# Performance work log

Hardware: AMD Instinct MI355X
Metric: run time of the kernel (lower is better)

Reference implementation:

```python
import jax, jax.numpy as jnp
import numpy as np

BSZ, IN_DIM, OUT_DIM = 512, 1024, 2048
M_AND = 5        # Anderson memory (self.m)
BETA = 1.0
LAM = 1e-4
ALPHA = 1.0
TOL = 1e-5
MAX_ITER = 50
M_MON = 1.0      # monotonicity parameter of MONSingleFc


def _multiply(A, B, z):
    # MONSingleFc.multiply: (1-m)z - z A^T A + z B^T - z B
    Az = z @ A.T
    return (1.0 - M_MON) * z - Az @ A + z @ B.T - z @ B


def _relu(z):
    return jnp.maximum(z, 0.0)


def _single_it(A, B, z, bias):
    zn = _multiply(A, B, z)
    zn = (1.0 - ALPHA) * z + ALPHA * (zn + bias)
    zn = _relu(zn)
    err = jnp.linalg.norm(zn - z) / (1e-6 + jnp.linalg.norm(zn))
    return zn, err


def _anderson_solve(A, B, bias):
    bsz, d = bias.shape
    dt = bias.dtype
    Z = jnp.zeros((bsz, M_AND, d), dt)
    F = jnp.zeros((bsz, M_AND, d), dt)
    z0 = jnp.zeros((bsz, d), dt)
    f0, _ = _single_it(A, B, z0, bias)
    F = F.at[:, 0].set(f0)
    Z = Z.at[:, 1].set(f0)
    f1, _ = _single_it(A, B, f0, bias)
    F = F.at[:, 1].set(f1)
    eye = jnp.eye(M_AND, dtype=dt)

    def cond(s):
        Z, F, it, err = s
        return (it < MAX_ITER) & (err > TOL)

    def body(s):
        Z, F, it, _ = s
        n = jnp.minimum(M_AND, it)
        mask = jnp.arange(M_AND) < n                         # active Anderson slots
        # For it < m the unused slots of Z and F are still zero, so G = F - Z
        # has zero rows there and GGt's Frobenius norm matches the :n slice.
        G = F - Z                                            # (bsz, m, d)
        GGt = jnp.einsum('bmd,bnd->bmn', G, G)
        nrm = jnp.linalg.norm(GGt.reshape(GGt.shape[0], -1), axis=-1)
        GGt = GGt / (nrm[:, None, None] + 1e-6)
        pair = mask[:, None] & mask[None, :]
        # identity padding on inactive slots keeps the solve well-posed and
        # yields alpha = 0 there, equivalent to slicing [:n+1, :n+1].
        Hb = jnp.where(pair, GGt + LAM * eye, eye)
        mk = mask.astype(dt)
        H = jnp.zeros((bsz, M_AND + 1, M_AND + 1), dt)
        H = H.at[:, 0, 1:].set(mk).at[:, 1:, 0].set(mk).at[:, 1:, 1:].set(Hb)
        y = jnp.zeros((bsz, M_AND + 1, 1), dt).at[:, 0, 0].set(1.0)
        alpha = jnp.linalg.solve(H, y)[:, 1:, 0]             # (bsz, m)
        z_new = BETA * jnp.einsum('bm,bmd->bd', alpha, F) \
              + (1.0 - BETA) * jnp.einsum('bm,bmd->bd', alpha, Z)
        slot = it % M_AND
        Z = Z.at[:, slot].set(z_new)
        zo, err = _single_it(A, B, z_new, bias)
        F = F.at[:, slot].set(zo)
        return Z, F, it + 1, err

    Z, F, it, err = jax.lax.while_loop(
        cond, body, (Z, F, jnp.array(2, jnp.int32), jnp.array(jnp.inf, dt)))
    slot = (it - 1) % M_AND
    return Z[:, slot]


def setup_inputs():
    key = jax.random.key(0)
    kx, ka, kb, kw, kub = jax.random.split(key, 5)
    s = 1.0 / np.sqrt(OUT_DIM).astype(np.float32)
    x = jax.random.normal(kx, (BSZ, IN_DIM), jnp.float32)
    # scaled so ||W|| < 1 -> forward-backward splitting converges (trained MON regime)
    A = 0.3 * s * jax.random.normal(ka, (OUT_DIM, OUT_DIM), jnp.float32)
    B = 0.1 * s * jax.random.normal(kb, (OUT_DIM, OUT_DIM), jnp.float32)
    U_W = (1.0 / np.sqrt(IN_DIM).astype(np.float32)) * jax.random.normal(kw, (OUT_DIM, IN_DIM), jnp.float32)
    U_b = 0.01 * jax.random.normal(kub, (OUT_DIM,), jnp.float32)
    return {"x": x, "A": A, "B": B, "U_W": U_W, "U_b": U_b}


def reference(x, A, B, U_W, U_b):
    bias = x @ U_W.T + U_b                       # linear_module.bias(x)
    z_star = _anderson_solve(A, B, bias)         # equilibrium (no-grad in torch)
    zn = _relu(_multiply(A, B, z_star) + bias)   # final full step: nonlin(linear(x, z*))
    return zn
```

## Files before the change

### kernel.cpp

```cpp
#include <hip/hip_runtime.h>
#include <hip/hip_bf16.h>
#include <math.h>

#define BSZ      512
#define IN_DIM   1024
#define OUT_DIM  2048
#define M_AND    5
#define LAM      1e-4f
#define TOL      1e-5f
#define MAX_ITER 50
#define SPLIT_IT 24
#define NBLK     256

typedef __bf16 bf16x8 __attribute__((ext_vector_type(8)));
typedef float  f32x4  __attribute__((ext_vector_type(4)));
typedef unsigned short u16x8 __attribute__((ext_vector_type(8)));
typedef unsigned short u16x4 __attribute__((ext_vector_type(4)));
typedef __hip_bfloat16 bf16;

#define GAS __attribute__((address_space(1)))
#define LAS __attribute__((address_space(3)))

union BU { bf16 b; unsigned short u; };

__device__ __forceinline__ float bf2f(unsigned short u) {
    union { unsigned int i; float f; } c; c.i = (unsigned int)u << 16; return c.f;
}
__device__ __forceinline__ unsigned short f2bf(float f) {
    BU t; t.b = __float2bfloat16(f); return t.u;
}

static constexpr size_t BIAS_B = 0;
static constexpr size_t F_B    = BIAS_B + (size_t)BSZ * OUT_DIM * 4;
static constexpr size_t G_B    = F_B    + (size_t)BSZ * M_AND * OUT_DIM * 4;
static constexpr size_t ZH_B   = G_B    + (size_t)BSZ * M_AND * OUT_DIM * 2;
static constexpr size_t ZL_B   = ZH_B   + (size_t)BSZ * OUT_DIM * 2;
static constexpr size_t XH_B   = ZL_B   + (size_t)BSZ * OUT_DIM * 2;
static constexpr size_t XL_B   = XH_B   + (size_t)BSZ * IN_DIM * 2;
static constexpr size_t UH_B   = XL_B   + (size_t)BSZ * IN_DIM * 2;
static constexpr size_t UL_B   = UH_B   + (size_t)OUT_DIM * IN_DIM * 2;
static constexpr size_t AT_B   = UL_B   + (size_t)OUT_DIM * IN_DIM * 2;
static constexpr size_t WT_B   = AT_B   + (size_t)OUT_DIM * OUT_DIM * 2;
static constexpr size_t RED_B  = WT_B   + (size_t)OUT_DIM * OUT_DIM * 2;
static constexpr size_t BAR_B  = RED_B  + 512;
static constexpr size_t CTR_B  = BAR_B  + 64;
static constexpr size_t FLAG_B = CTR_B  + 256;
static constexpr size_t CTRL_SZ = 512 + 64 + 256 + 16;

template<int ROUNDS>
__device__ __forceinline__ void stage_tile(const void* __restrict__ g0, int row_bytes,
                                           void* l0, int tid)
{
    #pragma unroll
    for (int q = 0; q < ROUNDS; ++q) {
        const int D   = q * 4096 + tid * 16;
        const int r   = D >> 7;
        const int cb  = D & 127;
        const int scb = cb ^ ((r & 7) << 4);
        const char* gsrc = (const char*)g0 + (size_t)r * row_bytes + scb;
        char* ldst = (char*)l0 + q * 4096 + (tid >> 6) * 1024;
        __builtin_amdgcn_global_load_lds((const GAS void*)gsrc, (LAS void*)ldst, 16, 0, 0);
    }
}

__device__ __forceinline__ bf16x8 read_frag(const void* tile, int row, int cb)
{
    return *(const bf16x8*)((const char*)tile + row * 128 + (cb ^ ((row & 7) << 4)));
}

__device__ __forceinline__ void gsync(unsigned int* bar)
{
    __syncthreads();
    if (threadIdx.x == 0) {
        __threadfence();
        const unsigned int g =
            __hip_atomic_load(&bar[1], __ATOMIC_ACQUIRE, __HIP_MEMORY_SCOPE_AGENT);
        const unsigned int a =
            __hip_atomic_fetch_add(&bar[0], 1u, __ATOMIC_ACQ_REL, __HIP_MEMORY_SCOPE_AGENT);
        if (a == NBLK - 1) {
            __hip_atomic_store(&bar[0], 0u, __ATOMIC_RELAXED, __HIP_MEMORY_SCOPE_AGENT);
            __hip_atomic_fetch_add(&bar[1], 1u, __ATOMIC_RELEASE, __HIP_MEMORY_SCOPE_AGENT);
        } else {
            while (__hip_atomic_load(&bar[1], __ATOMIC_ACQUIRE, __HIP_MEMORY_SCOPE_AGENT) == g)
                __builtin_amdgcn_s_sleep(1);
        }
        __threadfence();
    }
    __syncthreads();
}

__global__ __launch_bounds__(256)
void conv_hilo(const float* __restrict__ src, bf16* __restrict__ h, bf16* __restrict__ l)
{
    const size_t i4 = ((size_t)blockIdx.x * 256 + threadIdx.x) * 4;
    const float4 v = *(const float4*)&src[i4];
    const float vv[4] = {v.x, v.y, v.z, v.w};
    union { short4 s4; unsigned short u[4]; } ph, pl;
    #pragma unroll
    for (int j = 0; j < 4; ++j) {
        ph.u[j] = f2bf(vv[j]);
        pl.u[j] = f2bf(vv[j] - bf2f(ph.u[j]));
    }
    *(short4*)((char*)h + i4 * 2) = ph.s4;
    *(short4*)((char*)l + i4 * 2) = pl.s4;
}

__global__ __launch_bounds__(256)
void prep_at(const float* __restrict__ A, bf16* __restrict__ At)
{
    __shared__ float t[64][65];
    const int tid = threadIdx.x;
    const int k0 = blockIdx.y * 64, c0 = blockIdx.x * 64;
    const int cc = tid & 63, rr = tid >> 6;
    #pragma unroll
    for (int q = 0; q < 16; ++q)
        t[rr + 4 * q][cc] = A[(size_t)(k0 + rr + 4 * q) * OUT_DIM + c0 + cc];
    __syncthreads();
    #pragma unroll
    for (int q = 0; q < 16; ++q)
        At[(size_t)(c0 + rr + 4 * q) * OUT_DIM + k0 + cc] = __float2bfloat16(t[cc][rr + 4 * q]);
}

__global__ __launch_bounds__(256)
void w_mfma(const bf16* __restrict__ At, const float* __restrict__ Bm, bf16* __restrict__ Wt)
{
    __shared__ __align__(16) bf16 lds[2][2][64 * 64];
    const int tid = threadIdx.x;
    const int lane = tid & 63, wid = tid >> 6;
    const int wy = wid >> 1, wx = wid & 1;

    int bb = blockIdx.x;
    int ti = (int)((sqrtf(8.f * bb + 1.f) - 1.f) * 0.5f);
    while ((ti + 1) * (ti + 2) / 2 <= bb) ++ti;
    while (ti * (ti + 1) / 2 > bb) --ti;
    const int tj = bb - ti * (ti + 1) / 2;
    const int r0 = ti * 64, c0 = tj * 64;
    const bool diag = (ti == tj);

    f32x4 acc[2][2];
    #pragma unroll
    for (int i = 0; i < 2; ++i)
        #pragma unroll
        for (int j = 0; j < 2; ++j) acc[i][j] = 0;

    stage_tile<2>(At + (size_t)r0 * OUT_DIM, OUT_DIM * 2, lds[0][0], tid);
    stage_tile<2>(At + (size_t)c0 * OUT_DIM, OUT_DIM * 2, lds[0][1], tid);
    __syncthreads();
    int cur = 0;
    for (int t = 0; t < 32; ++t) {
        if (t + 1 < 32) {
            const int kk = (t + 1) * 64;
            stage_tile<2>(At + (size_t)r0 * OUT_DIM + kk, OUT_DIM * 2, lds[cur ^ 1][0], tid);
            stage_tile<2>(At + (size_t)c0 * OUT_DIM + kk, OUT_DIM * 2, lds[cur ^ 1][1], tid);
        }
        const bf16* Ta = lds[cur][0];
        const bf16* Tb = lds[cur][1];
        #pragma unroll
        for (int kf = 0; kf < 2; ++kf) {
            const int cb = kf * 64 + (lane >> 4) * 16;
            bf16x8 bfr[2];
            #pragma unroll
            for (int nj = 0; nj < 2; ++nj)
                bfr[nj] = read_frag(Tb, wx * 32 + nj * 16 + (lane & 15), cb);
            #pragma unroll
            for (int mi = 0; mi < 2; ++mi) {
                bf16x8 afr = read_frag(Ta, wy * 32 + mi * 16 + (lane & 15), cb);
                #pragma unroll
                for (int nj = 0; nj < 2; ++nj)
                    acc[mi][nj] = __builtin_amdgcn_mfma_f32_16x16x32_bf16(afr, bfr[nj], acc[mi][nj], 0, 0, 0);
            }
        }
        __syncthreads();
        cur ^= 1;
    }

    #pragma unroll
    for (int mi = 0; mi < 2; ++mi) {
        const int rb = r0 + wy * 32 + mi * 16 + (lane >> 4) * 4;
        #pragma unroll
        for (int nj = 0; nj < 2; ++nj) {
            const int c = c0 + wx * 32 + nj * 16 + (lane & 15);
            const float4 bc = *(const float4*)&Bm[(size_t)c * OUT_DIM + rb];
            const float bcv[4] = {bc.x, bc.y, bc.z, bc.w};
            union { short4 s4; unsigned short u[4]; } p;
            #pragma unroll
            for (int g = 0; g < 4; ++g) {
                const float a = acc[mi][nj][g];
                const float brc = Bm[(size_t)(rb + g) * OUT_DIM + c];
                const float w = bcv[g] - brc - a;
                p.u[g] = f2bf(w);
                if (!diag) {
                    const float wm = brc - bcv[g] - a;
                    *((unsigned short*)Wt + (size_t)(rb + g) * OUT_DIM + c) = f2bf(wm);
                }
            }
            *(short4*)((char*)Wt + ((size_t)c * OUT_DIM + rb) * 2) = p.s4;
        }
    }
}

__global__ __launch_bounds__(256)
void bias_mfma(const bf16* __restrict__ xh, const bf16* __restrict__ xl,
               const bf16* __restrict__ uh, const bf16* __restrict__ ul,
               const float* __restrict__ Ub, float* __restrict__ bias,
               float* __restrict__ F, unsigned short* __restrict__ G,
               unsigned short* __restrict__ zh, unsigned short* __restrict__ zl)
{
    __shared__ __align__(16) bf16 lds[2][4][64 * 64];
    const int tid = threadIdx.x;
    const int lane = tid & 63, wid = tid >> 6;
    const int wy = wid >> 1, wx = wid & 1;
    const int m0 = blockIdx.y * 64, n0 = blockIdx.x * 64;

    f32x4 acc[2][2];
    #pragma unroll
    for (int i = 0; i < 2; ++i)
        #pragma unroll
        for (int j = 0; j < 2; ++j) acc[i][j] = 0;

    stage_tile<2>(xh + (size_t)m0 * IN_DIM, IN_DIM * 2, lds[0][0], tid);
    stage_tile<2>(xl + (size_t)m0 * IN_DIM, IN_DIM * 2, lds[0][1], tid);
    stage_tile<2>(uh + (size_t)n0 * IN_DIM, IN_DIM * 2, lds[0][2], tid);
    stage_tile<2>(ul + (size_t)n0 * IN_DIM, IN_DIM * 2, lds[0][3], tid);
    __syncthreads();
    int cur = 0;
    for (int t = 0; t < 16; ++t) {
        if (t + 1 < 16) {
            const int kk = (t + 1) * 64;
            stage_tile<2>(xh + (size_t)m0 * IN_DIM + kk, IN_DIM * 2, lds[cur ^ 1][0], tid);
            stage_tile<2>(xl + (size_t)m0 * IN_DIM + kk, IN_DIM * 2, lds[cur ^ 1][1], tid);
            stage_tile<2>(uh + (size_t)n0 * IN_DIM + kk, IN_DIM * 2, lds[cur ^ 1][2], tid);
            stage_tile<2>(ul + (size_t)n0 * IN_DIM + kk, IN_DIM * 2, lds[cur ^ 1][3], tid);
        }
        const bf16* Txh = lds[cur][0];
        const bf16* Txl = lds[cur][1];
        const bf16* Tuh = lds[cur][2];
        const bf16* Tul = lds[cur][3];
        #pragma unroll
        for (int kf = 0; kf < 2; ++kf) {
            const int cb = kf * 64 + (lane >> 4) * 16;
            bf16x8 bh[2], bl[2];
            #pragma unroll
            for (int nj = 0; nj < 2; ++nj) {
                const int br = wx * 32 + nj * 16 + (lane & 15);
                bh[nj] = read_frag(Tuh, br, cb);
                bl[nj] = read_frag(Tul, br, cb);
            }
            #pragma unroll
            for (int mi = 0; mi < 2; ++mi) {
                const int ar = wy * 32 + mi * 16 + (lane & 15);
                bf16x8 ah = read_frag(Txh, ar, cb);
                bf16x8 al = read_frag(Txl, ar, cb);
                #pragma unroll
                for (int nj = 0; nj < 2; ++nj) {
                    acc[mi][nj] = __builtin_amdgcn_mfma_f32_16x16x32_bf16(ah, bh[nj], acc[mi][nj], 0, 0, 0);
                    acc[mi][nj] = __builtin_amdgcn_mfma_f32_16x16x32_bf16(ah, bl[nj], acc[mi][nj], 0, 0, 0);
                    acc[mi][nj] = __builtin_amdgcn_mfma_f32_16x16x32_bf16(al, bh[nj], acc[mi][nj], 0, 0, 0);
                }
            }
        }
        __syncthreads();
        cur ^= 1;
    }

    #pragma unroll
    for (int mi = 0; mi < 2; ++mi) {
        const int mb = m0 + wy * 32 + mi * 16 + (lane >> 4) * 4;
        #pragma unroll
        for (int nj = 0; nj < 2; ++nj) {
            const int n = n0 + wx * 32 + nj * 16 + (lane & 15);
            const float ub = Ub[n];
            #pragma unroll
            for (int g = 0; g < 4; ++g) {
                const int m = mb + g;
                const size_t idx = (size_t)m * OUT_DIM + n;
                const float v = acc[mi][nj][g] + ub;
                bias[idx] = v;
                const float f = fmaxf(v, 0.f);
                F[((size_t)m * M_AND + 0) * OUT_DIM + n] = f;
                G[((size_t)m * M_AND + 0) * OUT_DIM + n] = f2bf(f);
                const unsigned short h = f2bf(f);
                zh[idx] = h;
                zl[idx] = f2bf(f - bf2f(h));
            }
        }
    }
}

template<bool DO_ERR>
__device__ __forceinline__ void iter_core(
    const int m0, const int n0, const int tid,
    const unsigned short* __restrict__ zh, const unsigned short* __restrict__ zl,
    const bf16* __restrict__ Wt, const float* __restrict__ bias,
    float* __restrict__ F, unsigned short* __restrict__ G, float* __restrict__ out,
    float* red, bf16* lds_buf, const int slot, const int it)
{
    const int lane = tid & 63, wid = tid >> 6;
    const int wy = wid >> 1, wx = wid & 1;
    #define BUFP(c,i) (lds_buf + ((c) * 3 + (i)) * 4096)

    f32x4 acc[2][2];
    #pragma unroll
    for (int i = 0; i < 2; ++i)
        #pragma unroll
        for (int j = 0; j < 2; ++j) acc[i][j] = 0;

    stage_tile<2>(zh + (size_t)m0 * OUT_DIM, OUT_DIM * 2, BUFP(0, 0), tid);
    stage_tile<2>(zl + (size_t)m0 * OUT_DIM, OUT_DIM * 2, BUFP(0, 1), tid);
    stage_tile<2>(Wt + (size_t)n0 * OUT_DIM, OUT_DIM * 2, BUFP(0, 2), tid);
    __syncthreads();
    int cur = 0;
    for (int t = 0; t < 32; ++t) {
        if (t + 1 < 32) {
            const int kk = (t + 1) * 64;
            stage_tile<2>(zh + (size_t)m0 * OUT_DIM + kk, OUT_DIM * 2, BUFP(cur ^ 1, 0), tid);
            stage_tile<2>(zl + (size_t)m0 * OUT_DIM + kk, OUT_DIM * 2, BUFP(cur ^ 1, 1), tid);
            stage_tile<2>(Wt + (size_t)n0 * OUT_DIM + kk, OUT_DIM * 2, BUFP(cur ^ 1, 2), tid);
        }
        const bf16* Th = BUFP(cur, 0);
        const bf16* Tl = BUFP(cur, 1);
        const bf16* Tw = BUFP(cur, 2);
        #pragma unroll
        for (int kf = 0; kf < 2; ++kf) {
            const int cb = kf * 64 + (lane >> 4) * 16;
            bf16x8 bfr[2];
            #pragma unroll
            for (int nj = 0; nj < 2; ++nj)
                bfr[nj] = read_frag(Tw, wx * 32 + nj * 16 + (lane & 15), cb);
            #pragma unroll
            for (int mi = 0; mi < 2; ++mi) {
                const int rrow = wy * 32 + mi * 16 + (lane & 15);
                bf16x8 ah = read_frag(Th, rrow, cb);
                bf16x8 al = read_frag(Tl, rrow, cb);
                #pragma unroll
                for (int nj = 0; nj < 2; ++nj) {
                    acc[mi][nj] = __builtin_amdgcn_mfma_f32_16x16x32_bf16(ah, bfr[nj], acc[mi][nj], 0, 0, 0);
                    acc[mi][nj] = __builtin_amdgcn_mfma_f32_16x16x32_bf16(al, bfr[nj], acc[mi][nj], 0, 0, 0);
                }
            }
        }
        __syncthreads();
        cur ^= 1;
    }
    #undef BUFP

    float lnum = 0.f, lden = 0.f;
    #pragma unroll
    for (int mi = 0; mi < 2; ++mi) {
        const int mb = m0 + wy * 32 + mi * 16 + (lane >> 4) * 4;
        #pragma unroll
        for (int nj = 0; nj < 2; ++nj) {
            const int n = n0 + wx * 32 + nj * 16 + (lane & 15);
            #pragma unroll
            for (int g = 0; g < 4; ++g) {
                const int m = mb + g;
                const size_t idx = (size_t)m * OUT_DIM + n;
                float v = acc[mi][nj][g] + bias[idx];
                v = fmaxf(v, 0.f);
                const float zc = bf2f(zh[idx]) + bf2f(zl[idx]);
                const float gg = v - zc;
                F[((size_t)m * M_AND + slot) * OUT_DIM + n] = v;
                G[((size_t)m * M_AND + slot) * OUT_DIM + n] = f2bf(gg);
                out[idx] = v;
                if (DO_ERR) { lnum += gg * gg; lden += v * v; }
            }
        }
    }

    if (DO_ERR) {
        #pragma unroll
        for (int off = 32; off; off >>= 1) {
            lnum += __shfl_down(lnum, off);
            lden += __shfl_down(lden, off);
        }
        __shared__ float swn[4], swd[4];
        if ((tid & 63) == 0) { swn[tid >> 6] = lnum; swd[tid >> 6] = lden; }
        __syncthreads();
        if (tid == 0) {
            atomicAdd(&red[2 * it],     swn[0] + swn[1] + swn[2] + swn[3]);
            atomicAdd(&red[2 * it + 1], swd[0] + swd[1] + swd[2] + swd[3]);
        }
    }
}

template<bool DO_ERR>
__global__ __launch_bounds__(256)
void iter_mfma(const unsigned short* __restrict__ zh, const unsigned short* __restrict__ zl,
               const bf16* __restrict__ Wt, const float* __restrict__ bias,
               float* __restrict__ F, unsigned short* __restrict__ G, float* __restrict__ out,
               float* red, unsigned int* ctr, int* flag, int slot, int it)
{
    if (((volatile int*)flag)[0]) return;
    __shared__ __align__(16) bf16 lds_buf[2 * 3 * 4096];
    iter_core<DO_ERR>(blockIdx.y * 64, blockIdx.x * 64, threadIdx.x,
                      zh, zl, Wt, bias, F, G, out, red, lds_buf, slot, it);
    if (DO_ERR && threadIdx.x == 0) {
        __threadfence();
        const unsigned int done = atomicAdd(&ctr[it], 1u);
        if (done == 256 - 1) {
            const float num2 = ((volatile float*)red)[2 * it];
            const float den2 = ((volatile float*)red)[2 * it + 1];
            if (sqrtf(num2) <= TOL * (1e-6f + sqrtf(den2)))
                ((volatile int*)flag)[0] = 1;
        }
    }
}

__global__ __launch_bounds__(512)
void anderson_kernel(const float* __restrict__ F, const unsigned short* __restrict__ G,
                     unsigned short* __restrict__ zh, unsigned short* __restrict__ zl,
                     int* flag, int it)
{
    if (((volatile int*)flag)[0]) return;
    const int b = blockIdx.x;
    const int tid = threadIdx.x;
    const int lane = tid & 63, wid = tid >> 6;
    const int n = (it < M_AND) ? it : M_AND;
    const int c0 = tid * 4;
    const unsigned short* Gb = G + (size_t)b * M_AND * OUT_DIM;
    const float* Fb = F + (size_t)b * M_AND * OUT_DIM;

    float g[M_AND][4];
    float4 f[M_AND];
    #pragma unroll
    for (int m = 0; m < M_AND; ++m) {
        f[m] = *(const float4*)(Fb + (size_t)m * OUT_DIM + c0);
        if (m < n) {
            const u16x4 gv = *(const u16x4*)(Gb + (size_t)m * OUT_DIM + c0);
            #pragma unroll
            for (int q = 0; q < 4; ++q) g[m][q] = bf2f(gv[q]);
        } else {
            #pragma unroll
            for (int q = 0; q < 4; ++q) g[m][q] = 0.f;
        }
    }

    float dots[15];
    {
        int p = 0;
        #pragma unroll
        for (int i = 0; i < M_AND; ++i)
            #pragma unroll
            for (int j = i; j < M_AND; ++j) {
                float s = 0.f;
                #pragma unroll
                for (int q = 0; q < 4; ++q) s += g[i][q] * g[j][q];
                dots[p++] = s;
            }
    }

    __shared__ float sred[15][8];
    #pragma unroll
    for (int p = 0; p < 15; ++p) {
        float v = dots[p];
        #pragma unroll
        for (int off = 32; off; off >>= 1) v += __shfl_xor(v, off);
        if (lane == 0) sred[p][wid] = v;
    }
    __syncthreads();

    __shared__ float s_alpha[M_AND];
    if (tid == 0) {
        float GGm[M_AND][M_AND];
        int p = 0;
        for (int i = 0; i < M_AND; ++i)
            for (int j = i; j < M_AND; ++j) {
                float v = 0.f;
                for (int w = 0; w < 8; ++w) v += sred[p][w];
                GGm[i][j] = v; GGm[j][i] = v; ++p;
            }
        float fro = 0.f;
        for (int i = 0; i < M_AND; ++i)
            for (int j = 0; j < M_AND; ++j) fro += GGm[i][j] * GGm[i][j];
        const float inv = 1.f / (sqrtf(fro) + 1e-6f);

        float Mm[M_AND][M_AND];
        for (int i = 0; i < n; ++i)
            for (int j = 0; j < n; ++j)
                Mm[i][j] = GGm[i][j] * inv + (i == j ? LAM : 0.f);

        float L[M_AND][M_AND];
        for (int i = 0; i < n; ++i)
            for (int j = 0; j <= i; ++j) {
                float s = Mm[i][j];
                for (int k = 0; k < j; ++k) s -= L[i][k] * L[j][k];
                L[i][j] = (i == j) ? sqrtf(fmaxf(s, 1e-20f)) : s / L[j][j];
            }
        float y[M_AND], u[M_AND];
        for (int i = 0; i < n; ++i) {
            float s = 1.f;
            for (int k = 0; k < i; ++k) s -= L[i][k] * y[k];
            y[i] = s / L[i][i];
        }
        for (int i = n - 1; i >= 0; --i) {
            float s = y[i];
            for (int k = i + 1; k < n; ++k) s -= L[k][i] * u[k];
            u[i] = s / L[i][i];
        }
        float su = 0.f;
        for (int i = 0; i < n; ++i) su += u[i];
        const float isu = 1.f / su;
        for (int m = 0; m < M_AND; ++m) s_alpha[m] = (m < n) ? u[m] * isu : 0.f;
    }
    __syncthreads();

    float z[4] = {};
    #pragma unroll
    for (int m = 0; m < M_AND; ++m) {
        if (m < n) {
            const float a = s_alpha[m];
            z[0] += a * f[m].x; z[1] += a * f[m].y;
            z[2] += a * f[m].z; z[3] += a * f[m].w;
        }
    }
    u16x4 hv, lv;
    #pragma unroll
    for (int q = 0; q < 4; ++q) {
        const unsigned short h = f2bf(z[q]);
        hv[q] = h;
        lv[q] = f2bf(z[q] - bf2f(h));
    }
    *(u16x4*)(zh + (size_t)b * OUT_DIM + c0) = hv;
    *(u16x4*)(zl + (size_t)b * OUT_DIM + c0) = lv;
}

__global__ __launch_bounds__(256)
void tail_loop(unsigned short* zh, unsigned short* zl,
               const bf16* __restrict__ Wt, const float* __restrict__ bias,
               float* F, unsigned short* G, float* out,
               float* red, unsigned int* bar, int* flag)
{
    if (((volatile int*)flag)[0]) return;
    __shared__ __align__(16) bf16 lds_buf[2 * 3 * 4096];
    __shared__ float sred2[2][2][15];
    __shared__ float s_alpha[2][M_AND];
    const int bid = blockIdx.x, tid = threadIdx.x;

    for (int it = SPLIT_IT; it < MAX_ITER; ++it) {
        {
            const int half = tid >> 7, lt = tid & 127;
            const int r = bid * 2 + half;
            const int wv = lt >> 6;
            const unsigned short* Gb = G + (size_t)r * M_AND * OUT_DIM;
            const float* Fb = F + (size_t)r * M_AND * OUT_DIM;
            const int c0 = lt * 16;

            float g[M_AND][16];
            #pragma unroll
            for (int m = 0; m < M_AND; ++m) {
                const u16x8 ga = *(const u16x8*)(Gb + (size_t)m * OUT_DIM + c0);
                const u16x8 gb2 = *(const u16x8*)(Gb + (size_t)m * OUT_DIM + c0 + 8);
                #pragma unroll
                for (int q = 0; q < 8; ++q) { g[m][q] = bf2f(ga[q]); g[m][8 + q] = bf2f(gb2[q]); }
            }
            {
                int p = 0;
                #pragma unroll
                for (int i = 0; i < M_AND; ++i)
                    #pragma unroll
                    for (int j = i; j < M_AND; ++j) {
                        float s = 0.f;
                        #pragma unroll
                        for (int q = 0; q < 16; ++q) s += g[i][q] * g[j][q];
                        float v = s;
                        #pragma unroll
                        for (int off = 32; off; off >>= 1) v += __shfl_xor(v, off);
                        if ((lt & 63) == 0) sred2[half][wv][p] = v;
                        ++p;
                    }
            }
            __syncthreads();
            if (lt == 0) {
                float GGm[M_AND][M_AND];
                int p = 0;
                for (int i = 0; i < M_AND; ++i)
                    for (int j = i; j < M_AND; ++j) {
                        const float v = sred2[half][0][p] + sred2[half][1][p];
                        GGm[i][j] = v; GGm[j][i] = v; ++p;
                    }
                float fro = 0.f;
                for (int i = 0; i < M_AND; ++i)
                    for (int j = 0; j < M_AND; ++j) fro += GGm[i][j] * GGm[i][j];
                const float inv = 1.f / (sqrtf(fro) + 1e-6f);
                float Mm[M_AND][M_AND];
                for (int i = 0; i < M_AND; ++i)
                    for (int j = 0; j < M_AND; ++j)
                        Mm[i][j] = GGm[i][j] * inv + (i == j ? LAM : 0.f);
                float L[M_AND][M_AND];
                for (int i = 0; i < M_AND; ++i)
                    for (int j = 0; j <= i; ++j) {
                        float s = Mm[i][j];
                        for (int k = 0; k < j; ++k) s -= L[i][k] * L[j][k];
                        L[i][j] = (i == j) ? sqrtf(fmaxf(s, 1e-20f)) : s / L[j][j];
                    }
                float y[M_AND], u[M_AND];
                for (int i = 0; i < M_AND; ++i) {
                    float s = 1.f;
                    for (int k = 0; k < i; ++k) s -= L[i][k] * y[k];
                    y[i] = s / L[i][i];
                }
                for (int i = M_AND - 1; i >= 0; --i) {
                    float s = y[i];
                    for (int k = i + 1; k < M_AND; ++k) s -= L[k][i] * u[k];
                    u[i] = s / L[i][i];
                }
                float su = 0.f;
                for (int i = 0; i < M_AND; ++i) su += u[i];
                const float isu = 1.f / su;
                for (int m = 0; m < M_AND; ++m) s_alpha[half][m] = u[m] * isu;
            }
            __syncthreads();
            float z[16] = {};
            for (int m = 0; m < M_AND; ++m) {
                const float a = s_alpha[half][m];
                #pragma unroll
                for (int q = 0; q < 4; ++q) {
                    const float4 fv = *(const float4*)(Fb + (size_t)m * OUT_DIM + c0 + q * 4);
                    z[q * 4 + 0] += a * fv.x; z[q * 4 + 1] += a * fv.y;
                    z[q * 4 + 2] += a * fv.z; z[q * 4 + 3] += a * fv.w;
                }
            }
            u16x8 hv[2], lv[2];
            #pragma unroll
            for (int q = 0; q < 16; ++q) {
                const unsigned short h = f2bf(z[q]);
                hv[q >> 3][q & 7] = h;
                lv[q >> 3][q & 7] = f2bf(z[q] - bf2f(h));
            }
            const size_t base = (size_t)r * OUT_DIM + c0;
            *(u16x8*)(zh + base)     = hv[0];
            *(u16x8*)(zh + base + 8) = hv[1];
            *(u16x8*)(zl + base)     = lv[0];
            *(u16x8*)(zl + base + 8) = lv[1];
        }
        gsync(bar);
        iter_core<true>((bid >> 5) * 64, (bid & 31) * 64, tid,
                        zh, zl, Wt, bias, F, G, out, red, lds_buf, it % M_AND, it);
        gsync(bar);
        const float num2 = __hip_atomic_load(&red[2 * it], __ATOMIC_RELAXED, __HIP_MEMORY_SCOPE_AGENT);
        const float den2 = __hip_atomic_load(&red[2 * it + 1], __ATOMIC_RELAXED, __HIP_MEMORY_SCOPE_AGENT);
        if (sqrtf(num2) <= TOL * (1e-6f + sqrtf(den2))) break;
    }
}

extern "C" void kernel_launch(void* const* d_in, const int* in_sizes, int n_in,
                              void* d_out, int out_size, void* d_ws, size_t ws_size,
                              hipStream_t stream)
{
    const float* x  = (const float*)d_in[0];
    const float* A  = (const float*)d_in[1];
    const float* B  = (const float*)d_in[2];
    const float* UW = (const float*)d_in[3];
    const float* Ub = (const float*)d_in[4];
    float* out = (float*)d_out;
    char*  wsb = (char*)d_ws;

    float*          bias = (float*)(wsb + BIAS_B);
    float*          F    = (float*)(wsb + F_B);
    unsigned short* G    = (unsigned short*)(wsb + G_B);
    unsigned short* zh   = (unsigned short*)(wsb + ZH_B);
    unsigned short* zl   = (unsigned short*)(wsb + ZL_B);
    bf16*           xh   = (bf16*)(wsb + XH_B);
    bf16*           xl   = (bf16*)(wsb + XL_B);
    bf16*           uh   = (bf16*)(wsb + UH_B);
    bf16*           ul   = (bf16*)(wsb + UL_B);
    bf16*           At   = (bf16*)(wsb + AT_B);
    bf16*           Wt   = (bf16*)(wsb + WT_B);
    float*          red  = (float*)(wsb + RED_B);
    unsigned int*   bar  = (unsigned int*)(wsb + BAR_B);
    unsigned int*   ctr  = (unsigned int*)(wsb + CTR_B);
    int*            flag = (int*)(wsb + FLAG_B);

    hipMemsetAsync(wsb + RED_B, 0, CTRL_SZ, stream);

    conv_hilo<<<dim3(BSZ * IN_DIM / 1024),     256, 0, stream>>>(x,  xh, xl);
    conv_hilo<<<dim3(OUT_DIM * IN_DIM / 1024), 256, 0, stream>>>(UW, uh, ul);
    prep_at  <<<dim3(32, 32), 256, 0, stream>>>(A, At);
    w_mfma   <<<dim3(528), 256, 0, stream>>>(At, B, Wt);
    bias_mfma<<<dim3(32, 8), 256, 0, stream>>>(xh, xl, uh, ul, Ub, bias, F, G, zh, zl);

    iter_mfma<false><<<dim3(32, 8), 256, 0, stream>>>(zh, zl, Wt, bias, F, G, out,
                                                      red, ctr, flag, 1, 0);

    for (int it = 2; it < SPLIT_IT; ++it) {
        anderson_kernel<<<dim3(BSZ), 512, 0, stream>>>(F, G, zh, zl, flag, it);
        iter_mfma<true><<<dim3(32, 8), 256, 0, stream>>>(zh, zl, Wt, bias, F, G, out,
                                                         red, ctr, flag, it % M_AND, it);
    }
    tail_loop<<<dim3(NBLK), 256, 0, stream>>>(zh, zl, Wt, bias, F, G, out, red, bar, flag);
}
```

Baseline: 583.4 us.

## Triple-buffer iteration GEMM, swizzle tiles across XCDs, defer output write to final copy

The iteration GEMM moves from a double-buffered LDS pipeline to a three-stage one. It waits on vmcnt with a single barrier per k-step instead of two syncthreads, so global loads run further ahead of the MFMAs. Block-to-tile mapping is swizzled so each XCD works on a contiguous group of N columns, meant to improve L2 reuse of Wt. The per-iteration write of out is removed; a final_copy kernel reads the last F slot, recorded in fslot, and copies it to the output. This adds one extra kernel and depends on fslot being set correctly on every exit path.

```diff
diff --git a/kernel.cpp b/kernel.cpp
--- a/kernel.cpp
+++ b/kernel.cpp
@@ -20,6 +20,8 @@
 
 #define GAS __attribute__((address_space(1)))
 #define LAS __attribute__((address_space(3)))
+
+#define S_WAITCNT_VMCNT(N) asm volatile("s_waitcnt vmcnt(" #N ")" ::: "memory")
 
 union BU { bf16 b; unsigned short u; };
 
@@ -45,7 +47,8 @@
 static constexpr size_t BAR_B  = RED_B  + 512;
 static constexpr size_t CTR_B  = BAR_B  + 64;
 static constexpr size_t FLAG_B = CTR_B  + 256;
-static constexpr size_t CTRL_SZ = 512 + 64 + 256 + 16;
+static constexpr size_t FSLOT_B = FLAG_B + 16;
+static constexpr size_t CTRL_SZ = 512 + 64 + 256 + 16 + 16;
 
 template<int ROUNDS>
 __device__ __forceinline__ void stage_tile(const void* __restrict__ g0, int row_bytes,
@@ -292,12 +295,12 @@
     const int m0, const int n0, const int tid,
     const unsigned short* __restrict__ zh, const unsigned short* __restrict__ zl,
     const bf16* __restrict__ Wt, const float* __restrict__ bias,
-    float* __restrict__ F, unsigned short* __restrict__ G, float* __restrict__ out,
+    float* __restrict__ F, unsigned short* __restrict__ G,
     float* red, bf16* lds_buf, const int slot, const int it)
 {
     const int lane = tid & 63, wid = tid >> 6;
     const int wy = wid >> 1, wx = wid & 1;
-    #define BUFP(c,i) (lds_buf + ((c) * 3 + (i)) * 4096)
+    #define BUFP(s,i) (lds_buf + ((s) * 3 + (i)) * 4096)
 
     f32x4 acc[2][2];
     #pragma unroll
@@ -305,21 +308,22 @@
         #pragma unroll
         for (int j = 0; j < 2; ++j) acc[i][j] = 0;
 
-    stage_tile<2>(zh + (size_t)m0 * OUT_DIM, OUT_DIM * 2, BUFP(0, 0), tid);
-    stage_tile<2>(zl + (size_t)m0 * OUT_DIM, OUT_DIM * 2, BUFP(0, 1), tid);
-    stage_tile<2>(Wt + (size_t)n0 * OUT_DIM, OUT_DIM * 2, BUFP(0, 2), tid);
-    __syncthreads();
-    int cur = 0;
+    auto STAGE = [&](int s, int kk) {
+        stage_tile<2>(zh + (size_t)m0 * OUT_DIM + kk, OUT_DIM * 2, BUFP(s, 0), tid);
+        stage_tile<2>(zl + (size_t)m0 * OUT_DIM + kk, OUT_DIM * 2, BUFP(s, 1), tid);
+        stage_tile<2>(Wt + (size_t)n0 * OUT_DIM + kk, OUT_DIM * 2, BUFP(s, 2), tid);
+    };
+
+    STAGE(0, 0);
+    STAGE(1, 64);
     for (int t = 0; t < 32; ++t) {
-        if (t + 1 < 32) {
-            const int kk = (t + 1) * 64;
-            stage_tile<2>(zh + (size_t)m0 * OUT_DIM + kk, OUT_DIM * 2, BUFP(cur ^ 1, 0), tid);
-            stage_tile<2>(zl + (size_t)m0 * OUT_DIM + kk, OUT_DIM * 2, BUFP(cur ^ 1, 1), tid);
-            stage_tile<2>(Wt + (size_t)n0 * OUT_DIM + kk, OUT_DIM * 2, BUFP(cur ^ 1, 2), tid);
-        }
-        const bf16* Th = BUFP(cur, 0);
-        const bf16* Tl = BUFP(cur, 1);
-        const bf16* Tw = BUFP(cur, 2);
+        const int s = t % 3;
+        if (t + 2 < 32) { S_WAITCNT_VMCNT(6); } else { S_WAITCNT_VMCNT(0); }
+        __builtin_amdgcn_s_barrier();
+        if (t + 2 < 32) STAGE((t + 2) % 3, (t + 2) * 64);
+        const bf16* Th = BUFP(s, 0);
+        const bf16* Tl = BUFP(s, 1);
+        const bf16* Tw = BUFP(s, 2);
         #pragma unroll
         for (int kf = 0; kf < 2; ++kf) {
             const int cb = kf * 64 + (lane >> 4) * 16;
@@ -339,8 +343,6 @@
                 }
             }
         }
-        __syncthreads();
-        cur ^= 1;
     }
     #undef BUFP
 
@@ -361,7 +363,6 @@
                 const float gg = v - zc;
                 F[((size_t)m * M_AND + slot) * OUT_DIM + n] = v;
                 G[((size_t)m * M_AND + slot) * OUT_DIM + n] = f2bf(gg);
-                out[idx] = v;
                 if (DO_ERR) { lnum += gg * gg; lden += v * v; }
             }
         }
@@ -383,27 +384,46 @@
     }
 }
 
+__device__ __forceinline__ void swz_mn(int bid, int& m0, int& n0)
+{
+    const int xcd = bid & 7, sl = bid >> 3;
+    n0 = (xcd * 4 + (sl & 3)) * 64;
+    m0 = (sl >> 2) * 64;
+}
+
 template<bool DO_ERR>
 __global__ __launch_bounds__(256)
 void iter_mfma(const unsigned short* __restrict__ zh, const unsigned short* __restrict__ zl,
                const bf16* __restrict__ Wt, const float* __restrict__ bias,
-               float* __restrict__ F, unsigned short* __restrict__ G, float* __restrict__ out,
-               float* red, unsigned int* ctr, int* flag, int slot, int it)
+               float* __restrict__ F, unsigned short* __restrict__ G,
+               float* red, unsigned int* ctr, int* flag, int* fslot, int slot, int it)
 {
     if (((volatile int*)flag)[0]) return;
-    __shared__ __align__(16) bf16 lds_buf[2 * 3 * 4096];
-    iter_core<DO_ERR>(blockIdx.y * 64, blockIdx.x * 64, threadIdx.x,
-                      zh, zl, Wt, bias, F, G, out, red, lds_buf, slot, it);
+    __shared__ __align__(16) bf16 lds_buf[3 * 3 * 4096];
+    int m0, n0;
+    swz_mn(blockIdx.x, m0, n0);
+    iter_core<DO_ERR>(m0, n0, threadIdx.x, zh, zl, Wt, bias, F, G, red, lds_buf, slot, it);
     if (DO_ERR && threadIdx.x == 0) {
         __threadfence();
         const unsigned int done = atomicAdd(&ctr[it], 1u);
         if (done == 256 - 1) {
+            ((volatile int*)fslot)[0] = slot;
             const float num2 = ((volatile float*)red)[2 * it];
             const float den2 = ((volatile float*)red)[2 * it + 1];
             if (sqrtf(num2) <= TOL * (1e-6f + sqrtf(den2)))
                 ((volatile int*)flag)[0] = 1;
         }
     }
+}
+
+__global__ __launch_bounds__(256)
+void final_copy(const float* __restrict__ F, const int* __restrict__ fslot,
+                float* __restrict__ out)
+{
+    const int s = ((volatile const int*)fslot)[0];
+    const size_t i4 = ((size_t)blockIdx.x * 256 + threadIdx.x) * 4;
+    const int m = (int)(i4 >> 11), n = (int)(i4 & 2047);
+    *(float4*)&out[i4] = *(const float4*)&F[((size_t)m * M_AND + s) * OUT_DIM + n];
 }
 
 __global__ __launch_bounds__(512)
@@ -527,14 +547,16 @@
 __global__ __launch_bounds__(256)
 void tail_loop(unsigned short* zh, unsigned short* zl,
                const bf16* __restrict__ Wt, const float* __restrict__ bias,
-               float* F, unsigned short* G, float* out,
-               float* red, unsigned int* bar, int* flag)
+               float* F, unsigned short* G,
+               float* red, unsigned int* bar, int* flag, int* fslot)
 {
     if (((volatile int*)flag)[0]) return;
-    __shared__ __align__(16) bf16 lds_buf[2 * 3 * 4096];
+    __shared__ __align__(16) bf16 lds_buf[3 * 3 * 4096];
     __shared__ float sred2[2][2][15];
     __shared__ float s_alpha[2][M_AND];
     const int bid = blockIdx.x, tid = threadIdx.x;
+    int m0, n0;
+    swz_mn(bid, m0, n0);
 
     for (int it = SPLIT_IT; it < MAX_ITER; ++it) {
         {
@@ -634,9 +656,9 @@
             *(u16x8*)(zl + base + 8) = lv[1];
         }
         gsync(bar);
-        iter_core<true>((bid >> 5) * 64, (bid & 31) * 64, tid,
-                        zh, zl, Wt, bias, F, G, out, red, lds_buf, it % M_AND, it);
+        iter_core<true>(m0, n0, tid, zh, zl, Wt, bias, F, G, red, lds_buf, it % M_AND, it);
         gsync(bar);
+        if (bid == 0 && tid == 0) ((volatile int*)fslot)[0] = it % M_AND;
         const float num2 = __hip_atomic_load(&red[2 * it], __ATOMIC_RELAXED, __HIP_MEMORY_SCOPE_AGENT);
         const float den2 = __hip_atomic_load(&red[2 * it + 1], __ATOMIC_RELAXED, __HIP_MEMORY_SCOPE_AGENT);
         if (sqrtf(num2) <= TOL * (1e-6f + sqrtf(den2))) break;
@@ -670,6 +692,7 @@
     unsigned int*   bar  = (unsigned int*)(wsb + BAR_B);
     unsigned int*   ctr  = (unsigned int*)(wsb + CTR_B);
     int*            flag = (int*)(wsb + FLAG_B);
+    int*            fslot= (int*)(wsb + FSLOT_B);
 
     hipMemsetAsync(wsb + RED_B, 0, CTRL_SZ, stream);
 
@@ -679,13 +702,14 @@
     w_mfma   <<<dim3(528), 256, 0, stream>>>(At, B, Wt);
     bias_mfma<<<dim3(32, 8), 256, 0, stream>>>(xh, xl, uh, ul, Ub, bias, F, G, zh, zl);
 
-    iter_mfma<false><<<dim3(32, 8), 256, 0, stream>>>(zh, zl, Wt, bias, F, G, out,
-                                                      red, ctr, flag, 1, 0);
+    iter_mfma<false><<<dim3(NBLK), 256, 0, stream>>>(zh, zl, Wt, bias, F, G,
+                                                     red, ctr, flag, fslot, 1, 0);
 
     for (int it = 2; it < SPLIT_IT; ++it) {
         anderson_kernel<<<dim3(BSZ), 512, 0, stream>>>(F, G, zh, zl, flag, it);
-        iter_mfma<true><<<dim3(32, 8), 256, 0, stream>>>(zh, zl, Wt, bias, F, G, out,
-                                                         red, ctr, flag, it % M_AND, it);
-    }
-    tail_loop<<<dim3(NBLK), 256, 0, stream>>>(zh, zl, Wt, bias, F, G, out, red, bar, flag);
-}
+        iter_mfma<true><<<dim3(NBLK), 256, 0, stream>>>(zh, zl, Wt, bias, F, G,
+                                                        red, ctr, flag, fslot, it % M_AND, it);
+    }
+    tail_loop<<<dim3(NBLK), 256, 0, stream>>>(zh, zl, Wt, bias, F, G, red, bar, flag, fslot);
+    final_copy<<<dim3(BSZ * OUT_DIM / 1024), 256, 0, stream>>>(F, fslot, out);
+}
```

Result: faster. 569.9 us (-2.3%).
